# Kernel optimization log

Measured on AMD Instinct MI355X. Metric: run time of the kernel, lower is better.

## Reference

```python
import jax, jax.numpy as jnp
import numpy as np
from jax import lax

B, W, H, C = 32, 512, 512, 3
PSF = 32


def setup_inputs() -> dict:
    key = jax.random.key(0)
    k1, k2, k3 = jax.random.split(key, 3)
    observed_images = jax.random.normal(k1, (B, W, H, C), dtype=jnp.float32)
    # trainable vars of the keras model (estimated_image would be initialized to
    # mean(observed) on the first call; we treat it as a free parameter)
    estimated_image = jax.random.normal(k2, (W, H, C), dtype=jnp.float32)
    point_spread_functions = jax.random.normal(k3, (B, PSF, PSF, 1, C), dtype=jnp.float32) * 0.05
    return {
        "observed_images": observed_images,
        "estimated_image": estimated_image,
        "point_spread_functions": point_spread_functions,
    }


def _per_example_conv(img_nhwc, psf_hwio):
    # img_nhwc: [1, W, H, C]; psf_hwio: [k, k, 1, C] -> grouped (depthwise) conv,
    # feature_group_count = C, matching tf.nn.conv2d's grouped-conv semantics.
    out = lax.conv_general_dilated(
        img_nhwc, psf_hwio,
        window_strides=(1, 1), padding="SAME",
        dimension_numbers=("NHWC", "HWIO", "NHWC"),
        feature_group_count=img_nhwc.shape[-1],
    )
    return out[0]  # [W, H, C]


def reference(observed_images, estimated_image, point_spread_functions):
    img = estimated_image[None]  # [1, W, H, C], shared across batch
    # vmap over the per-example PSF kernels replaces the python loop of B conv2d calls
    predicted = jax.vmap(lambda psf: _per_example_conv(img, psf))(point_spread_functions)
    # predicted: [B, W, H, C]
    loss = jnp.mean((observed_images - predicted) ** 2)
    return predicted, loss
```

## Files before the change

kernel.cpp:

```cpp
#include <hip/hip_runtime.h>
#include <hip/hip_bf16.h>

#define BATCH 32
#define WDIM 512
#define HDIM 512
#define CDIM 3
#define KPSF 32
#define NPRED (BATCH*WDIM*HDIM*CDIM)

#define TW 56
#define TH 63
#define TE (TW*TH)
#define TALL (TW*TH*CDIM)

typedef __bf16 bf16x8 __attribute__((ext_vector_type(8)));
typedef float floatx16 __attribute__((ext_vector_type(16)));
typedef float fx4 __attribute__((ext_vector_type(4)));

__device__ __forceinline__ void barrier_lgkm() {
    __asm__ volatile("s_waitcnt lgkmcnt(0)\n\ts_barrier" ::: "memory");
}

__global__ __launch_bounds__(64) void pack_psf(const float* __restrict__ psf,
                                               __bf16* __restrict__ dst,
                                               float* __restrict__ loss) {
    if (blockIdx.x == 0 && threadIdx.x == 0) *loss = 0.f;
    int idx = blockIdx.x;
    int h = idx & 1;
    int j = (idx >> 1) & 31;
    int c = idx >> 6;
    int lane = threadIdx.x;
    int b = lane & 31;
    int q = lane >> 5;
    bf16x8 v;
#pragma unroll
    for (int t = 0; t < 8; ++t) {
        int i = 16*h + 8*q + t;
        v[t] = (__bf16)psf[((size_t)(b*KPSF + i)*KPSF + j)*CDIM + c];
    }
    *(bf16x8*)(dst + (size_t)(idx*64 + lane)*8) = v;
}

__global__ __launch_bounds__(192, 4) void conv_mfma(
    const float* __restrict__ obs,
    const float* __restrict__ img,
    const __bf16* __restrict__ psfA,
    float* __restrict__ out)
{
    __shared__ __align__(16) unsigned char smem[CDIM*TE*2];
    __bf16 (*sImg)[TE] = (__bf16 (*)[TE])smem;
    float* sOut = (float*)smem;

    const int tid  = threadIdx.x;
    const int lane = tid & 63;
    const int c    = tid >> 6;
    const int n    = lane & 31;
    const int q    = lane >> 5;

    const int bx = blockIdx.x;
    const int r8 = bx & 7;
    const int g  = (bx >> 3) & 15;
    const int yt = bx >> 7;
    const int x0 = g*32 + r8;
    const int ytile = yt*32;

    const bool interior = (x0 >= 15) && (x0 <= WDIM - 41) &&
                          (ytile >= 15) && (ytile <= HDIM - 48);
    if (interior) {
        const int col0 = (ytile - 15)*3;
        const int p2 = col0 & 3;
        const float* gb = img + (size_t)(x0 - 15)*(HDIM*CDIM) + (col0 - p2);
#pragma unroll 2
        for (int f = tid; f < 56*48; f += 192) {
            int r = f / 48;
            int v = f - r*48;
            fx4 val = *(const fx4*)(gb + (size_t)r*(HDIM*CDIM) + 4*v);
            int d = 4*v - p2;
#pragma unroll
            for (int u = 0; u < 4; ++u) {
                int dd = d + u;
                if (dd >= 0 && dd < 189) {
                    int yl = (dd*171) >> 9;
                    int cc = dd - 3*yl;
                    sImg[cc][yl*TW + r] = (__bf16)val[u];
                }
            }
        }
    } else {
#pragma unroll 4
        for (int e = tid; e < TALL; e += 192) {
            int xl = e / (TH*CDIM);
            int rr = e - xl*(TH*CDIM);
            int yl = rr / 3;
            int cc = rr - yl*3;
            int xg = x0 + xl - 15;
            int yg = ytile + yl - 15;
            float v = 0.f;
            if ((unsigned)xg < WDIM && (unsigned)yg < HDIM)
                v = img[((size_t)xg*HDIM + yg)*CDIM + cc];
            sImg[cc][yl*TW + xl] = (__bf16)v;
        }
    }
    __syncthreads();

    floatx16 acc[4] = {};
    const __bf16* pA = psfA + (size_t)c*(KPSF*2*64*8) + (size_t)lane*8;
    const __bf16* sI = (const __bf16*)&sImg[c][q*8];

    bf16x8 A0 = *(const bf16x8*)(pA);
    bf16x8 A1 = *(const bf16x8*)(pA + 512);
#pragma unroll 2
    for (int j = 0; j < 32; ++j) {
        bf16x8 cA0 = A0, cA1 = A1;
        if (j < 31) {
            A0 = *(const bf16x8*)(pA + (size_t)(j+1)*1024);
            A1 = *(const bf16x8*)(pA + (size_t)(j+1)*1024 + 512);
        }
        const __bf16* rowp = sI + (n + j)*TW;
        bf16x8 C[6];
#pragma unroll
        for (int rr = 0; rr < 6; ++rr)
            C[rr] = *(const bf16x8*)(rowp + rr*8);
#pragma unroll
        for (int s = 0; s < 4; ++s) {
            acc[s] = __builtin_amdgcn_mfma_f32_32x32x16_bf16(cA0, C[s],   acc[s], 0, 0, 0);
            acc[s] = __builtin_amdgcn_mfma_f32_32x32x16_bf16(cA1, C[s+2], acc[s], 0, 0, 0);
        }
    }

    float ls = 0.f;
    unsigned base[4];
#pragma unroll
    for (int k = 0; k < 4; ++k) {
        int f = tid + 192*k;
        int fb = f / 24;
        int r4 = (f - fb*24) * 4;
        base[k] = ((unsigned)(fb*WDIM + x0)*HDIM + (unsigned)ytile)*CDIM + r4;
    }
    fx4 ob[4];
#pragma unroll
    for (int k = 0; k < 4; ++k)
        ob[k] = __builtin_nontemporal_load((const fx4*)&obs[base[k]]);

#pragma unroll
    for (int t = 0; t < 4; ++t) {
        barrier_lgkm();
#pragma unroll
        for (int rr = 0; rr < 16; ++rr) {
            int b = (rr & 3) + 8*(rr >> 2) + 4*q;
            sOut[(b*32 + n)*3 + c] = acc[t][rr];
        }
        barrier_lgkm();
        fx4 cur[4];
#pragma unroll
        for (int k = 0; k < 4; ++k) cur[k] = ob[k];
        if (t < 3) {
#pragma unroll
            for (int k = 0; k < 4; ++k)
                ob[k] = __builtin_nontemporal_load(
                    (const fx4*)&obs[base[k] + (unsigned)(t+1)*8*HDIM*CDIM]);
        }
#pragma unroll
        for (int k = 0; k < 4; ++k) {
            fx4 p = *(const fx4*)&sOut[4*(tid + 192*k)];
            __builtin_nontemporal_store(p, (fx4*)&out[base[k] + (unsigned)t*8*HDIM*CDIM]);
            fx4 d = cur[k] - p;
            ls += d[0]*d[0] + d[1]*d[1] + d[2]*d[2] + d[3]*d[3];
        }
    }

#pragma unroll
    for (int m = 32; m >= 1; m >>= 1) ls += __shfl_xor(ls, m, 64);
    if (lane == 0) atomicAdd(out + NPRED, ls * (1.0f/(float)NPRED));
}

extern "C" void kernel_launch(void* const* d_in, const int* in_sizes, int n_in,
                              void* d_out, int out_size, void* d_ws, size_t ws_size,
                              hipStream_t stream) {
    const float* obs = (const float*)d_in[0];
    const float* img = (const float*)d_in[1];
    const float* psf = (const float*)d_in[2];
    float* out = (float*)d_out;
    __bf16* psfA = (__bf16*)d_ws;

    pack_psf<<<192, 64, 0, stream>>>(psf, psfA, out + NPRED);
    conv_mfma<<<2048, 192, 0, stream>>>(obs, img, psfA, out);
}
```

Measured before the change: 262.9 us.

## Stream PSF operands through a per-wave LDS ring via global_load_lds

The bf16 PSF A-operands were fetched from global memory straight into registers, one j-step ahead. They are now brought in by asynchronous global-to-LDS loads into a 5-slot ring buffer per wave, prefetching four steps ahead and gated by vmcnt waits. The aim is to hide global load latency in the MFMA loop and cut register pressure. In exchange, LDS use grows to about 52 KB per block and the launch-bounds occupancy hint drops from 4 to 3 blocks per CU, which reduces latency hiding elsewhere.

New measurement: 258.0 us. No clear change (-1.9%).

```diff
diff --git a/kernel.cpp b/kernel.cpp
--- a/kernel.cpp
+++ b/kernel.cpp
@@ -13,12 +13,22 @@
 #define TE (TW*TH)
 #define TALL (TW*TH*CDIM)
 
+#define RING_OFF 21168
+#define RING_PER_WAVE 10240
+#define LDS_BYTES (RING_OFF + CDIM*RING_PER_WAVE)
+
 typedef __bf16 bf16x8 __attribute__((ext_vector_type(8)));
 typedef float floatx16 __attribute__((ext_vector_type(16)));
 typedef float fx4 __attribute__((ext_vector_type(4)));
 
 __device__ __forceinline__ void barrier_lgkm() {
     __asm__ volatile("s_waitcnt lgkmcnt(0)\n\ts_barrier" ::: "memory");
+}
+
+__device__ __forceinline__ void ldsA(const void* g, void* l) {
+    __builtin_amdgcn_global_load_lds(
+        (const __attribute__((address_space(1))) void*)g,
+        (__attribute__((address_space(3))) void*)l, 16, 0, 0);
 }
 
 __global__ __launch_bounds__(64) void pack_psf(const float* __restrict__ psf,
@@ -41,13 +51,13 @@
     *(bf16x8*)(dst + (size_t)(idx*64 + lane)*8) = v;
 }
 
-__global__ __launch_bounds__(192, 4) void conv_mfma(
+__global__ __launch_bounds__(192, 3) void conv_mfma(
     const float* __restrict__ obs,
     const float* __restrict__ img,
     const __bf16* __restrict__ psfA,
     float* __restrict__ out)
 {
-    __shared__ __align__(16) unsigned char smem[CDIM*TE*2];
+    __shared__ __align__(16) unsigned char smem[LDS_BYTES];
     __bf16 (*sImg)[TE] = (__bf16 (*)[TE])smem;
     float* sOut = (float*)smem;
 
@@ -63,6 +73,15 @@
     const int yt = bx >> 7;
     const int x0 = g*32 + r8;
     const int ytile = yt*32;
+
+    const char* gA   = (const char*)psfA + (size_t)c*65536 + (size_t)(lane*16);
+    char* ringU      = (char*)smem + RING_OFF + c*RING_PER_WAVE;
+    const char* ringL = ringU + lane*16;
+#pragma unroll
+    for (int s0 = 0; s0 < 4; ++s0) {
+        ldsA(gA + s0*2048,        ringU + s0*2048);
+        ldsA(gA + s0*2048 + 1024, ringU + s0*2048 + 1024);
+    }
 
     const bool interior = (x0 >= 15) && (x0 <= WDIM - 41) &&
                           (ytile >= 15) && (ytile <= HDIM - 48);
@@ -101,21 +120,18 @@
             sImg[cc][yl*TW + xl] = (__bf16)v;
         }
     }
-    __syncthreads();
+    barrier_lgkm();
 
     floatx16 acc[4] = {};
-    const __bf16* pA = psfA + (size_t)c*(KPSF*2*64*8) + (size_t)lane*8;
     const __bf16* sI = (const __bf16*)&sImg[c][q*8];
 
-    bf16x8 A0 = *(const bf16x8*)(pA);
-    bf16x8 A1 = *(const bf16x8*)(pA + 512);
+    asm volatile("s_waitcnt vmcnt(6)" ::: "memory");
+    bf16x8 Ac0 = *(const bf16x8*)(ringL);
+    bf16x8 Ac1 = *(const bf16x8*)(ringL + 1024);
+    int rd = 2048;
+    int wr = 8192;
 #pragma unroll 2
     for (int j = 0; j < 32; ++j) {
-        bf16x8 cA0 = A0, cA1 = A1;
-        if (j < 31) {
-            A0 = *(const bf16x8*)(pA + (size_t)(j+1)*1024);
-            A1 = *(const bf16x8*)(pA + (size_t)(j+1)*1024 + 512);
-        }
         const __bf16* rowp = sI + (n + j)*TW;
         bf16x8 C[6];
 #pragma unroll
@@ -123,9 +139,18 @@
             C[rr] = *(const bf16x8*)(rowp + rr*8);
 #pragma unroll
         for (int s = 0; s < 4; ++s) {
-            acc[s] = __builtin_amdgcn_mfma_f32_32x32x16_bf16(cA0, C[s],   acc[s], 0, 0, 0);
-            acc[s] = __builtin_amdgcn_mfma_f32_32x32x16_bf16(cA1, C[s+2], acc[s], 0, 0, 0);
-        }
+            acc[s] = __builtin_amdgcn_mfma_f32_32x32x16_bf16(Ac0, C[s],   acc[s], 0, 0, 0);
+            acc[s] = __builtin_amdgcn_mfma_f32_32x32x16_bf16(Ac1, C[s+2], acc[s], 0, 0, 0);
+        }
+        int js = ((j + 4) & 31)*2048;
+        ldsA(gA + js,        ringU + wr);
+        ldsA(gA + js + 1024, ringU + wr + 1024);
+        asm volatile("s_waitcnt vmcnt(6)" ::: "memory");
+        bf16x8 An0 = *(const bf16x8*)(ringL + rd);
+        bf16x8 An1 = *(const bf16x8*)(ringL + rd + 1024);
+        rd += 2048; if (rd == RING_PER_WAVE) rd = 0;
+        wr += 2048; if (wr == RING_PER_WAVE) wr = 0;
+        Ac0 = An0; Ac1 = An1;
     }
 
     float ls = 0.f;
```

## Use persistent blocks with a rolling circular LDS image window over y-tiles

Applied to the files above, without the earlier changes.

Each block now covers a 64-wide x strip of 8 interleaved rows and walks four 32-column y tiles, keeping the image halo in a 64-row circular LDS buffer. Only 32 new halo rows are loaded per step, prefetched into registers while the MFMAs run. The PSF fragments are double-buffered across two taps, and observed-image loads are split around the MFMA loop. This cuts redundant halo loads and brings the grid down to 256 blocks with occupancy 1, at the risk of fewer waves to hide latency and much higher register pressure.

Result: slower. 275.3 us (+4.7%).

```diff
diff --git a/kernel.cpp b/kernel.cpp
--- a/kernel.cpp
+++ b/kernel.cpp
@@ -8,10 +8,11 @@
 #define KPSF 32
 #define NPRED (BATCH*WDIM*HDIM*CDIM)
 
-#define TW 56
-#define TH 63
-#define TE (TW*TH)
-#define TALL (TW*TH*CDIM)
+#define TW 88
+#define NROW 64
+#define TE (TW*NROW)
+#define SOUT_OFF (CDIM*TE*2)
+#define LDS_BYTES (SOUT_OFF + 12288)
 
 typedef __bf16 bf16x8 __attribute__((ext_vector_type(8)));
 typedef float floatx16 __attribute__((ext_vector_type(16)));
@@ -41,15 +42,15 @@
     *(bf16x8*)(dst + (size_t)(idx*64 + lane)*8) = v;
 }
 
-__global__ __launch_bounds__(192, 4) void conv_mfma(
+__global__ __launch_bounds__(192, 1) void conv_mfma(
     const float* __restrict__ obs,
     const float* __restrict__ img,
     const __bf16* __restrict__ psfA,
     float* __restrict__ out)
 {
-    __shared__ __align__(16) unsigned char smem[CDIM*TE*2];
-    __bf16 (*sImg)[TE] = (__bf16 (*)[TE])smem;
-    float* sOut = (float*)smem;
+    __shared__ __align__(16) unsigned char smem[LDS_BYTES];
+    __bf16* sim  = (__bf16*)smem;
+    float*  sOut = (float*)(smem + SOUT_OFF);
 
     const int tid  = threadIdx.x;
     const int lane = tid & 63;
@@ -59,113 +60,157 @@
 
     const int bx = blockIdx.x;
     const int r8 = bx & 7;
-    const int g  = (bx >> 3) & 15;
-    const int yt = bx >> 7;
-    const int x0 = g*32 + r8;
-    const int ytile = yt*32;
-
-    const bool interior = (x0 >= 15) && (x0 <= WDIM - 41) &&
-                          (ytile >= 15) && (ytile <= HDIM - 48);
-    if (interior) {
-        const int col0 = (ytile - 15)*3;
-        const int p2 = col0 & 3;
-        const float* gb = img + (size_t)(x0 - 15)*(HDIM*CDIM) + (col0 - p2);
-#pragma unroll 2
-        for (int f = tid; f < 56*48; f += 192) {
-            int r = f / 48;
-            int v = f - r*48;
-            fx4 val = *(const fx4*)(gb + (size_t)r*(HDIM*CDIM) + 4*v);
-            int d = 4*v - p2;
-#pragma unroll
-            for (int u = 0; u < 4; ++u) {
-                int dd = d + u;
-                if (dd >= 0 && dd < 189) {
-                    int yl = (dd*171) >> 9;
-                    int cc = dd - 3*yl;
-                    sImg[cc][yl*TW + r] = (__bf16)val[u];
-                }
-            }
-        }
-    } else {
-#pragma unroll 4
-        for (int e = tid; e < TALL; e += 192) {
-            int xl = e / (TH*CDIM);
-            int rr = e - xl*(TH*CDIM);
-            int yl = rr / 3;
-            int cc = rr - yl*3;
-            int xg = x0 + xl - 15;
-            int yg = ytile + yl - 15;
-            float v = 0.f;
-            if ((unsigned)xg < WDIM && (unsigned)yg < HDIM)
-                v = img[((size_t)xg*HDIM + yg)*CDIM + cc];
-            sImg[cc][yl*TW + xl] = (__bf16)v;
-        }
-    }
-    __syncthreads();
-
-    floatx16 acc[4] = {};
-    const __bf16* pA = psfA + (size_t)c*(KPSF*2*64*8) + (size_t)lane*8;
-    const __bf16* sI = (const __bf16*)&sImg[c][q*8];
-
-    bf16x8 A0 = *(const bf16x8*)(pA);
-    bf16x8 A1 = *(const bf16x8*)(pA + 512);
-#pragma unroll 2
-    for (int j = 0; j < 32; ++j) {
-        bf16x8 cA0 = A0, cA1 = A1;
-        if (j < 31) {
-            A0 = *(const bf16x8*)(pA + (size_t)(j+1)*1024);
-            A1 = *(const bf16x8*)(pA + (size_t)(j+1)*1024 + 512);
-        }
-        const __bf16* rowp = sI + (n + j)*TW;
-        bf16x8 C[6];
-#pragma unroll
-        for (int rr = 0; rr < 6; ++rr)
-            C[rr] = *(const bf16x8*)(rowp + rr*8);
-#pragma unroll
-        for (int s = 0; s < 4; ++s) {
-            acc[s] = __builtin_amdgcn_mfma_f32_32x32x16_bf16(cA0, C[s],   acc[s], 0, 0, 0);
-            acc[s] = __builtin_amdgcn_mfma_f32_32x32x16_bf16(cA1, C[s+2], acc[s], 0, 0, 0);
-        }
-    }
-
-    float ls = 0.f;
-    unsigned base[4];
+    const int g  = (bx >> 3) & 7;
+    const int yq = bx >> 6;
+    const int x0 = g*64 + r8;
+    const int Y0 = yq*128;
+
+    for (int e = tid; e < 88*189; e += 192) {
+        int xl = e / 189;
+        int r  = e - xl*189;
+        int yl = r / 3;
+        int cc = r - 3*yl;
+        int x = x0 - 15 + xl;
+        int y = Y0 - 15 + yl;
+        float v = 0.f;
+        if ((unsigned)x < WDIM && (unsigned)y < HDIM)
+            v = img[((size_t)x*HDIM + y)*CDIM + cc];
+        sim[cc*TE + ((y + 512) & 63)*TW + xl] = (__bf16)v;
+    }
+
+    const char* gA = (const char*)psfA + (size_t)c*65536 + (size_t)(lane*16);
+
+    unsigned baseNoY[4];
 #pragma unroll
     for (int k = 0; k < 4; ++k) {
         int f = tid + 192*k;
         int fb = f / 24;
         int r4 = (f - fb*24) * 4;
-        base[k] = ((unsigned)(fb*WDIM + x0)*HDIM + (unsigned)ytile)*CDIM + r4;
-    }
-    fx4 ob[4];
-#pragma unroll
-    for (int k = 0; k < 4; ++k)
-        ob[k] = __builtin_nontemporal_load((const fx4*)&obs[base[k]]);
-
-#pragma unroll
-    for (int t = 0; t < 4; ++t) {
+        baseNoY[k] = (unsigned)fb*(WDIM*HDIM*CDIM) + (unsigned)x0*(HDIM*CDIM) + r4;
+    }
+
+    float ls = 0.f;
+    fx4 rl[11];
+
+#pragma unroll 1
+    for (int tt = 0; tt < 4; ++tt) {
+        const int Y = Y0 + 32*tt;
+
+        if (tt > 0) {
+            const int y0r = Y + 16;
+#pragma unroll
+            for (int i = 0; i < 11; ++i) {
+                int f = tid + 192*i;
+                int col = f / 24;
+                int v4  = f - col*24;
+#pragma unroll
+                for (int u = 0; u < 4; ++u) {
+                    int dd = 4*v4 + u;
+                    int yl = dd / 3;
+                    int cc = dd - 3*yl;
+                    int y  = y0r + yl;
+                    float val = (y < HDIM) ? rl[i][u] : 0.f;
+                    sim[cc*TE + (y & 63)*TW + col] = (__bf16)val;
+                }
+            }
+        }
         barrier_lgkm();
-#pragma unroll
-        for (int rr = 0; rr < 16; ++rr) {
-            int b = (rr & 3) + 8*(rr >> 2) + 4*q;
-            sOut[(b*32 + n)*3 + c] = acc[t][rr];
-        }
-        barrier_lgkm();
-        fx4 cur[4];
-#pragma unroll
-        for (int k = 0; k < 4; ++k) cur[k] = ob[k];
-        if (t < 3) {
+
+        if (tt < 3) {
+            const int y0n = Y + 48;
+#pragma unroll
+            for (int i = 0; i < 11; ++i) {
+                int f = tid + 192*i;
+                int col = f / 24;
+                int v4  = f - col*24;
+                int x = x0 - 15 + col;
+                rl[i] = fx4{0.f, 0.f, 0.f, 0.f};
+                if ((unsigned)x < WDIM)
+                    rl[i] = *(const fx4*)&img[((size_t)x*HDIM + y0n)*CDIM + 4*v4];
+            }
+        }
+
+        unsigned baseT[4];
+#pragma unroll
+        for (int k = 0; k < 4; ++k) baseT[k] = baseNoY[k] + (unsigned)(Y*CDIM);
+        fx4 obA[4][4], obB[4][4];
+#pragma unroll
+        for (int s = 0; s < 4; ++s)
 #pragma unroll
             for (int k = 0; k < 4; ++k)
-                ob[k] = __builtin_nontemporal_load(
-                    (const fx4*)&obs[base[k] + (unsigned)(t+1)*8*HDIM*CDIM]);
-        }
-#pragma unroll
-        for (int k = 0; k < 4; ++k) {
-            fx4 p = *(const fx4*)&sOut[4*(tid + 192*k)];
-            __builtin_nontemporal_store(p, (fx4*)&out[base[k] + (unsigned)t*8*HDIM*CDIM]);
-            fx4 d = cur[k] - p;
-            ls += d[0]*d[0] + d[1]*d[1] + d[2]*d[2] + d[3]*d[3];
+                obA[s][k] = __builtin_nontemporal_load(
+                    (const fx4*)&obs[baseT[k] + (unsigned)s*8*HDIM*CDIM]);
+
+        floatx16 acc[8] = {};
+        const int KT = (Y + 497) & 63;
+        const __bf16* sIc = sim + c*TE + q*8;
+
+        bf16x8 Aa0 = *(const bf16x8*)(gA);
+        bf16x8 Aa1 = *(const bf16x8*)(gA + 1024);
+        bf16x8 Ab0 = *(const bf16x8*)(gA + 2048);
+        bf16x8 Ab1 = *(const bf16x8*)(gA + 3072);
+#pragma unroll 1
+        for (int jj = 0; jj < 32; jj += 2) {
+            int jn2 = ((jj + 2) & 31) * 2048;
+            bf16x8 Ac0 = *(const bf16x8*)(gA + jn2);
+            bf16x8 Ac1 = *(const bf16x8*)(gA + jn2 + 1024);
+            {
+                int slot = (KT + n + jj) & 63;
+                const __bf16* rowp = sIc + slot*TW;
+                bf16x8 C[10];
+#pragma unroll
+                for (int rr = 0; rr < 10; ++rr)
+                    C[rr] = *(const bf16x8*)(rowp + rr*8);
+#pragma unroll
+                for (int s = 0; s < 8; ++s) {
+                    acc[s] = __builtin_amdgcn_mfma_f32_32x32x16_bf16(Aa0, C[s],   acc[s], 0, 0, 0);
+                    acc[s] = __builtin_amdgcn_mfma_f32_32x32x16_bf16(Aa1, C[s+2], acc[s], 0, 0, 0);
+                }
+            }
+            int jn3 = ((jj + 3) & 31) * 2048;
+            bf16x8 Ad0 = *(const bf16x8*)(gA + jn3);
+            bf16x8 Ad1 = *(const bf16x8*)(gA + jn3 + 1024);
+            {
+                int slot = (KT + n + jj + 1) & 63;
+                const __bf16* rowp = sIc + slot*TW;
+                bf16x8 C[10];
+#pragma unroll
+                for (int rr = 0; rr < 10; ++rr)
+                    C[rr] = *(const bf16x8*)(rowp + rr*8);
+#pragma unroll
+                for (int s = 0; s < 8; ++s) {
+                    acc[s] = __builtin_amdgcn_mfma_f32_32x32x16_bf16(Ab0, C[s],   acc[s], 0, 0, 0);
+                    acc[s] = __builtin_amdgcn_mfma_f32_32x32x16_bf16(Ab1, C[s+2], acc[s], 0, 0, 0);
+                }
+            }
+            Aa0 = Ac0; Aa1 = Ac1; Ab0 = Ad0; Ab1 = Ad1;
+        }
+
+#pragma unroll
+        for (int s = 0; s < 4; ++s)
+#pragma unroll
+            for (int k = 0; k < 4; ++k)
+                obB[s][k] = __builtin_nontemporal_load(
+                    (const fx4*)&obs[baseT[k] + (unsigned)(s+4)*8*HDIM*CDIM]);
+
+#pragma unroll
+        for (int s = 0; s < 8; ++s) {
+            barrier_lgkm();
+#pragma unroll
+            for (int rr = 0; rr < 16; ++rr) {
+                int b = (rr & 3) + 8*(rr >> 2) + 4*q;
+                sOut[(b*32 + n)*3 + c] = acc[s][rr];
+            }
+            barrier_lgkm();
+#pragma unroll
+            for (int k = 0; k < 4; ++k) {
+                fx4 p = *(const fx4*)&sOut[4*(tid + 192*k)];
+                __builtin_nontemporal_store(
+                    p, (fx4*)&out[baseT[k] + (unsigned)s*8*HDIM*CDIM]);
+                fx4 o = (s < 4) ? obA[s][k] : obB[s-4][k];
+                fx4 d = o - p;
+                ls += d[0]*d[0] + d[1]*d[1] + d[2]*d[2] + d[3]*d[3];
+            }
         }
     }
 
@@ -184,5 +229,5 @@
     __bf16* psfA = (__bf16*)d_ws;
 
     pack_psf<<<192, 64, 0, stream>>>(psf, psfA, out + NPRED);
-    conv_mfma<<<2048, 192, 0, stream>>>(obs, img, psfA, out);
-}
+    conv_mfma<<<256, 192, 0, stream>>>(obs, img, psfA, out);
+}
```
